# Performance work log

Hardware: AMD Instinct MI355X
Metric: run time of the kernel (lower is better)

## Reference

```python
import jax, jax.numpy as jnp
from jax import lax
import numpy as np

N_DFT = 1024
N_HOP = 256
N_FILTER = N_DFT // 2 + 1  # 513
AMIN = 1e-10
DYNAMIC_RANGE = 80.0


def _make_dft_kernels(n_dft):
    """Real/imag DFT kernels with periodic Hann window, shape (n_dft, 1, n_filter) for WIO conv."""
    nb = n_dft // 2 + 1
    t = np.arange(n_dft)
    w = np.arange(nb) * 2.0 * np.pi / float(n_dft)
    real = np.cos(w[:, None] * t[None, :])           # (nb, n_dft)
    imag = -np.sin(w[:, None] * t[None, :])
    # scipy periodic ('fftbins=True') hann window
    win = 0.5 - 0.5 * np.cos(2.0 * np.pi * t / float(n_dft))
    real = (real * win).T[:, None, :]                # (n_dft, 1, nb) = (W, I, O)
    imag = (imag * win).T[:, None, :]
    return real.astype(np.float32), imag.astype(np.float32)


def setup_inputs() -> dict:
    key = jax.random.key(0)
    x = jax.random.normal(key, (32, 2, 262144), dtype=jnp.float32)  # (batch, n_ch, len_src)
    kr, ki = _make_dft_kernels(N_DFT)
    return {"x": x, "k_real": jnp.asarray(kr), "k_imag": jnp.asarray(ki)}


def reference(x, k_real, k_imag):
    B, CH, L = x.shape
    xm = x.reshape(B * CH, L, 1)  # treat each audio channel as an independent mono signal
    dn = ("NWC", "WIO", "NWC")
    conv = lambda k: lax.conv_general_dilated(
        xm, k, window_strides=(N_HOP,), padding="SAME", dimension_numbers=dn
    )
    # power spectrogram: real^2 + imag^2 -> (B*CH, n_frame, n_filter)
    power = conv(k_real) ** 2 + conv(k_imag) ** 2
    n_frame = power.shape[1]
    # -> (B, n_filter, n_frame, CH)  (channels_last image format)
    spec = power.reshape(B, CH, n_frame, N_FILTER).transpose(0, 3, 2, 1)
    # power_spectrogram == 2.0, so no pow; return_decibel_spectrogram == True:
    log_spec = 10.0 * jnp.log10(jnp.maximum(spec, AMIN))
    log_spec = log_spec - jnp.max(log_spec, axis=(1, 2, 3), keepdims=True)
    return jnp.maximum(log_spec, -DYNAMIC_RANGE)
```

## Files before the change

### kernel.cpp

```cpp
#include <hip/hip_runtime.h>
#include <math.h>

namespace {
constexpr int NDFT   = 1024;
constexpr int NHOP   = 256;
constexpr int NFILT  = 513;
constexpr int LSRC   = 262144;
constexpr int NFRAME = 1024;
constexpr int PAD_L  = 384;
constexpr long PER_B = (long)NFILT * NFRAME * 2;

constexpr int KT2 = 16;
constexpr int CHUNK_US = 8192;
constexpr size_t WSB2_BYTES = (size_t)8 * KT2 * CHUNK_US * 2;
constexpr size_t PLANE_ELEMS_PER_SIG = 1024 * 512;

constexpr int KT1 = 32;
constexpr size_t WS_B_BYTES = (size_t)8 * KT1 * CHUNK_US * 2;
}

using short8 = __attribute__((ext_vector_type(8))) short;
using f32x4  = __attribute__((ext_vector_type(4))) float;

__device__ __forceinline__ unsigned int f2key(float f) {
    unsigned int u = __float_as_uint(f);
    return (u & 0x80000000u) ? ~u : (u | 0x80000000u);
}
__device__ __forceinline__ float key2f(unsigned int k) {
    return (k & 0x80000000u) ? __uint_as_float(k ^ 0x80000000u) : __uint_as_float(~k);
}
__device__ __forceinline__ unsigned short bf16rn(float v) {
    unsigned int u = __float_as_uint(v);
    return (unsigned short)((u + 0x7fffu + ((u >> 16) & 1u)) >> 16);
}

__global__ void zero_ws(unsigned int* __restrict__ w) {
    if (threadIdx.x < 32) w[threadIdx.x] = 0u;
}

__global__ __launch_bounds__(256) void fold_split(
    const float* __restrict__ x,
    unsigned short* __restrict__ sH, unsigned short* __restrict__ sL,
    unsigned short* __restrict__ dH, unsigned short* __restrict__ dL,
    int sig0)
{
    const int floc = blockIdx.x * 4 + (threadIdx.x >> 6);
    const int grp  = threadIdx.x & 63;
    const int sig  = sig0 + (floc >> 10);
    const int fl   = floc & 1023;
    const long sbase = (long)sig * LSRC;
    const int st   = fl * NHOP - PAD_L;
    const int s0   = grp * 8;

    const float xmid = x[sbase + st + 512];

    float fw[8], bw[8];
    if (fl >= 2 && fl <= 1021) {
        const float4 a0 = *reinterpret_cast<const float4*>(x + sbase + st + s0);
        const float4 a1 = *reinterpret_cast<const float4*>(x + sbase + st + s0 + 4);
        fw[0]=a0.x; fw[1]=a0.y; fw[2]=a0.z; fw[3]=a0.w;
        fw[4]=a1.x; fw[5]=a1.y; fw[6]=a1.z; fw[7]=a1.w;
        const long q0 = sbase + st + 1017 - s0;
        const float4 b0 = *reinterpret_cast<const float4*>(x + q0 - 1);
        const float4 b1 = *reinterpret_cast<const float4*>(x + q0 + 3);
        const float  b2 = x[q0 + 7];
        const float va[8] = {b0.y, b0.z, b0.w, b1.x, b1.y, b1.z, b1.w, b2};
        #pragma unroll
        for (int j = 0; j < 8; ++j) bw[j] = va[7 - j];
    } else {
        #pragma unroll
        for (int j = 0; j < 8; ++j) {
            const int s = s0 + j;
            const int p1 = st + s;
            const int p2 = st + 1024 - s;
            fw[j] = ((unsigned)p1 < (unsigned)LSRC) ? x[sbase + p1] : 0.0f;
            bw[j] = ((unsigned)p2 < (unsigned)LSRC) ? x[sbase + p2] : 0.0f;
        }
    }

    union { unsigned short u[8]; uint4 v; } shv, slv, dhv, dlv;
    #pragma unroll
    for (int j = 0; j < 8; ++j) {
        float x1 = fw[j], x2 = bw[j];
        if (j == 0 && s0 == 0) { x1 = xmid; x2 = 0.0f; }
        const float sm = x1 + x2;
        const float df = x1 - x2;
        const unsigned short h1 = bf16rn(sm);
        shv.u[j] = h1;
        slv.u[j] = bf16rn(sm - __uint_as_float((unsigned int)h1 << 16));
        const unsigned short h2 = bf16rn(df);
        dhv.u[j] = h2;
        dlv.u[j] = bf16rn(df - __uint_as_float((unsigned int)h2 << 16));
    }
    const size_t wo = (size_t)floc * 512 + s0;
    *reinterpret_cast<uint4*>(sH + wo) = shv.v;
    *reinterpret_cast<uint4*>(sL + wo) = slv.v;
    *reinterpret_cast<uint4*>(dH + wo) = dhv.v;
    *reinterpret_cast<uint4*>(dL + wo) = dlv.v;
}

__global__ __launch_bounds__(256) void build_B2(const float* __restrict__ kr,
                                                const float* __restrict__ ki,
                                                unsigned short* __restrict__ wsB)
{
    const int nt = blockIdx.x >> 4;
    const int kt = blockIdx.x & 15;
    unsigned short* chunk = wsB + (size_t)blockIdx.x * CHUNK_US;
    const int col = threadIdx.x >> 1;
    const int h   = threadIdx.x & 1;
    const int bin = nt * 64 + (col & 63);
    const float* src = (col < 64) ? kr : ki;
    #pragma unroll
    for (int j = 0; j < 4; ++j) {
        const int sl = h * 4 + j;
        const int c  = sl & 3;
        union { unsigned short u[8]; uint4 v; } pk;
        #pragma unroll
        for (int i = 0; i < 8; ++i) {
            const int s = kt * 32 + c * 8 + i;
            const int t = (s == 0) ? 512 : s;
            const float v = src[t * NFILT + bin];
            const unsigned short hi = bf16rn(v);
            pk.u[i] = h ? bf16rn(v - __uint_as_float((unsigned int)hi << 16)) : hi;
        }
        *reinterpret_cast<uint4*>(&chunk[col * 64 + ((sl ^ (col & 7)) << 3)]) = pk.v;
    }
}

__global__ __launch_bounds__(256, 2) void spec_gemm2(
    const unsigned short* __restrict__ sH, const unsigned short* __restrict__ sL,
    const unsigned short* __restrict__ dH, const unsigned short* __restrict__ dL,
    const unsigned short* __restrict__ wsB,
    float* __restrict__ out, unsigned int* __restrict__ wmax,
    int sig0, int nsig)
{
    __shared__ unsigned short smem[24576];

    const int tid  = threadIdx.x;
    const int lane = tid & 63, w = tid >> 6;
    const int wm = w & 1, wn = w >> 1;
    const int l15 = lane & 15, l16 = lane >> 4;

    const int phys = blockIdx.x;
    const int xcd  = phys & 7, slot = phys >> 3;
    const int nt   = slot & 7;
    const int mt   = xcd * nsig + (slot >> 3);
    const int sig  = sig0 + (mt >> 3);
    const int f0   = (mt & 7) * 128;
    const unsigned short* bchunks = wsB + (size_t)nt * KT2 * CHUNK_US;

    const unsigned short* __restrict__ pH = wn ? dH : sH;
    const unsigned short* __restrict__ pL = wn ? dL : sL;

    const int rl = lane >> 3, jj = lane & 7;
    const int q  = jj ^ rl;
    const unsigned short* apl = (q < 4) ? pH : pL;
    const unsigned short* agsrc[8];
    #pragma unroll
    for (int i = 0; i < 8; ++i)
        agsrc[i] = apl + (size_t)(mt * 128 + wm * 64 + i * 8 + rl) * 512 + (q & 3) * 8;

    unsigned short* Areg  = smem + wn * 12288;
    unsigned short* Breg  = Areg + 8192;
    unsigned short* aldst = Areg + wm * 4096;
    unsigned short* bldst = Breg + wm * 2048;

    f32x4 acc[4][4];
    #pragma unroll
    for (int i = 0; i < 4; ++i)
        #pragma unroll
        for (int j = 0; j < 4; ++j)
            #pragma unroll
            for (int r = 0; r < 4; ++r) acc[i][j][r] = 0.0f;

    #define STAGE(ktv)                                                         \
        {                                                                      \
            _Pragma("unroll")                                                  \
            for (int i = 0; i < 8; ++i)                                        \
                __builtin_amdgcn_global_load_lds(                              \
                    (const __attribute__((address_space(1))) unsigned int*)(agsrc[i] + (ktv) * 32), \
                    (__attribute__((address_space(3))) unsigned int*)(aldst + i * 512), \
                    16, 0, 0);                                                 \
            const unsigned short* gBs = bchunks + (size_t)(ktv) * CHUNK_US + wn * 4096 + wm * 2048; \
            _Pragma("unroll")                                                  \
            for (int i = 0; i < 4; ++i)                                        \
                __builtin_amdgcn_global_load_lds(                              \
                    (const __attribute__((address_space(1))) unsigned int*)(gBs + i * 512 + lane * 8), \
                    (__attribute__((address_space(3))) unsigned int*)(bldst + i * 512), \
                    16, 0, 0);                                                 \
        }

    #define COMPUTE()                                                          \
        {                                                                      \
            short8 ah[4], al[4], bh[4], bl[4];                                 \
            _Pragma("unroll")                                                  \
            for (int mf = 0; mf < 4; ++mf) {                                   \
                const int row = wm * 64 + mf * 16 + l15;                       \
                const unsigned short* ab = Areg + row * 64;                    \
                ah[mf] = *reinterpret_cast<const short8*>(ab + ((l16 ^ (row & 7)) << 3));        \
                al[mf] = *reinterpret_cast<const short8*>(ab + (((4 + l16) ^ (row & 7)) << 3));  \
            }                                                                  \
            _Pragma("unroll")                                                  \
            for (int nf = 0; nf < 4; ++nf) {                                   \
                const int coll = nf * 16 + l15;                                \
                const unsigned short* bb = Breg + coll * 64;                   \
                bh[nf] = *reinterpret_cast<const short8*>(bb + ((l16 ^ (coll & 7)) << 3));       \
                bl[nf] = *reinterpret_cast<const short8*>(bb + (((4 + l16) ^ (coll & 7)) << 3)); \
            }                                                                  \
            __builtin_amdgcn_s_setprio(1);                                     \
            _Pragma("unroll")                                                  \
            for (int nf = 0; nf < 4; ++nf)                                     \
                _Pragma("unroll")                                              \
                for (int mf = 0; mf < 4; ++mf) {                               \
                    acc[mf][nf] = __builtin_amdgcn_mfma_f32_16x16x32_bf16(ah[mf], bh[nf], acc[mf][nf], 0, 0, 0); \
                    acc[mf][nf] = __builtin_amdgcn_mfma_f32_16x16x32_bf16(al[mf], bh[nf], acc[mf][nf], 0, 0, 0); \
                    acc[mf][nf] = __builtin_amdgcn_mfma_f32_16x16x32_bf16(ah[mf], bl[nf], acc[mf][nf], 0, 0, 0); \
                }                                                              \
            __builtin_amdgcn_s_setprio(0);                                     \
        }

    #pragma unroll 1
    for (int kt = 0; kt < KT2; ++kt) {
        STAGE(kt)
        __syncthreads();
        COMPUTE()
        __syncthreads();
    }
    #undef STAGE
    #undef COMPUTE

    if (wn == 0) {
        #pragma unroll
        for (int mf = 0; mf < 4; ++mf)
            #pragma unroll
            for (int nf = 0; nf < 4; ++nf) {
                const int binl = nf * 16 + l15;
                #pragma unroll
                for (int r = 0; r < 4; ++r) {
                    const int row = wm * 64 + mf * 16 + l16 * 4 + r;
                    const float v = acc[mf][nf][r];
                    smem[row * 68 + binl] = bf16rn(v * v);
                }
            }
    }
    __syncthreads();
    if (wn == 1) {
        const int batch = sig >> 1, ch = sig & 1;
        float lmax = -3.0e38f;
        #pragma unroll
        for (int mf = 0; mf < 4; ++mf)
            #pragma unroll
            for (int nf = 0; nf < 4; ++nf) {
                const int binl = nf * 16 + l15;
                const int bin  = nt * 64 + binl;
                #pragma unroll
                for (int r = 0; r < 4; ++r) {
                    const int row = wm * 64 + mf * 16 + l16 * 4 + r;
                    const float v = acc[mf][nf][r];
                    const float re2 = __uint_as_float((unsigned int)smem[row * 68 + binl] << 16);
                    const float p = re2 + v * v;
                    const float d = 10.0f * log10f(fmaxf(p, 1e-10f));
                    const int frame = f0 + row;
                    out[((long)(batch * NFILT + bin) * NFRAME + frame) * 2 + ch] = d;
                    lmax = fmaxf(lmax, d);
                }
            }
        #pragma unroll
        for (int off = 32; off > 0; off >>= 1) lmax = fmaxf(lmax, __shfl_xor(lmax, off));
        if (lane == 0) atomicMax(&wmax[batch], f2key(lmax));
    }
}

__global__ __launch_bounds__(256) void build_B(const float* __restrict__ kr,
                                               const float* __restrict__ ki,
                                               unsigned short* __restrict__ wsB)
{
    const int nt = blockIdx.x >> 5;
    const int kt = blockIdx.x & 31;
    unsigned short* chunk = wsB + (size_t)blockIdx.x * CHUNK_US;
    const int col = threadIdx.x >> 1;
    const int h   = threadIdx.x & 1;
    const int bin = nt * 64 + (col >> 1);
    const float* src = (col & 1) ? ki : kr;
    #pragma unroll
    for (int j = 0; j < 4; ++j) {
        const int sl = h * 4 + j;
        const int c  = sl & 3;
        union { unsigned short u[8]; uint4 v; } pk;
        #pragma unroll
        for (int i = 0; i < 8; ++i) {
            const int t = kt * 32 + c * 8 + i;
            const float v = src[t * NFILT + bin];
            const unsigned short hi = bf16rn(v);
            pk.u[i] = h ? bf16rn(v - __uint_as_float((unsigned int)hi << 16)) : hi;
        }
        *reinterpret_cast<uint4*>(&chunk[col * 64 + ((sl ^ (col & 7)) << 3)]) = pk.v;
    }
}

__global__ __launch_bounds__(256, 2) void spec_gemm_mid(
    const float* __restrict__ x, const unsigned short* __restrict__ wsB,
    float* __restrict__ out, unsigned int* __restrict__ wmax)
{
    __shared__ unsigned short Ad[2][128][64];
    __shared__ unsigned short Bd[2][128][64];

    const int tid  = threadIdx.x;
    const int lane = tid & 63, w = tid >> 6;
    const int wm = w >> 1, wn = w & 1;
    const int l15 = lane & 15, l16 = lane >> 4;
    const int mt = blockIdx.x, nt = blockIdx.y;
    const int sig = mt >> 3, f0 = (mt & 7) * 128;
    const long sb = (long)sig * LSRC;

    const int arow = tid >> 1, ac2 = tid & 1;
    const int abase_p = (f0 + arow) * NHOP - PAD_L + ac2 * 16;
    const unsigned short* bchunks = wsB + (size_t)nt * KT1 * CHUNK_US;

    f32x4 acc[4][4];
    #pragma unroll
    for (int i = 0; i < 4; ++i)
        #pragma unroll
        for (int j = 0; j < 4; ++j)
            #pragma unroll
            for (int r = 0; r < 4; ++r) acc[i][j][r] = 0.0f;

    float va[16];

    #define LOAD_A(ktv)                                                        \
        {                                                                      \
            const int p0 = abase_p + (ktv) * 32;                               \
            if (p0 >= 0 && p0 + 16 <= LSRC) {                                  \
                *reinterpret_cast<float4*>(&va[0])  = *reinterpret_cast<const float4*>(x + sb + p0);      \
                *reinterpret_cast<float4*>(&va[4])  = *reinterpret_cast<const float4*>(x + sb + p0 + 4);  \
                *reinterpret_cast<float4*>(&va[8])  = *reinterpret_cast<const float4*>(x + sb + p0 + 8);  \
                *reinterpret_cast<float4*>(&va[12]) = *reinterpret_cast<const float4*>(x + sb + p0 + 12); \
            } else {                                                           \
                _Pragma("unroll")                                              \
                for (int i = 0; i < 16; ++i) {                                 \
                    const int p = p0 + i;                                      \
                    va[i] = (p >= 0 && p < LSRC) ? x[sb + p] : 0.0f;           \
                }                                                              \
            }                                                                  \
        }

    #define LOAD_B(ktv, nb)                                                    \
        {                                                                      \
            const char* g = (const char*)(bchunks + (size_t)(ktv) * CHUNK_US); \
            char* l = (char*)&Bd[nb][0][0];                                    \
            _Pragma("unroll")                                                  \
            for (int i = 0; i < 4; ++i) {                                      \
                const int off = i * 4096 + w * 1024;                           \
                __builtin_amdgcn_global_load_lds(                              \
                    (const __attribute__((address_space(1))) unsigned int*)(g + off + lane * 16), \
                    (__attribute__((address_space(3))) unsigned int*)(l + off), \
                    16, 0, 0);                                                 \
            }                                                                  \
        }

    #define WRITE_A(nb)                                                       \
        {                                                                      \
            unsigned short* ab = &Ad[nb][arow][0];                             \
            _Pragma("unroll")                                                  \
            for (int j = 0; j < 2; ++j) {                                      \
                union { unsigned short u[8]; uint4 v; } hv, lv;                \
                _Pragma("unroll")                                              \
                for (int i = 0; i < 8; ++i) {                                  \
                    const float vv = va[j * 8 + i];                            \
                    const unsigned short hi = bf16rn(vv);                      \
                    hv.u[i] = hi;                                              \
                    lv.u[i] = bf16rn(vv - __uint_as_float((unsigned int)hi << 16)); \
                }                                                              \
                const int c = ac2 * 2 + j;                                     \
                *reinterpret_cast<uint4*>(ab + (((c) ^ (arow & 7)) << 3))     = hv.v; \
                *reinterpret_cast<uint4*>(ab + (((4 + c) ^ (arow & 7)) << 3)) = lv.v; \
            }                                                                  \
        }

    LOAD_A(0)
    LOAD_B(0, 0)
    WRITE_A(0)
    __syncthreads();

    #pragma unroll 1
    for (int kt = 0; kt < KT1; ++kt) {
        const int cur = kt & 1, nxt = cur ^ 1;
        const bool pf = (kt + 1 < KT1);
        if (pf) {
            LOAD_A(kt + 1)
            LOAD_B(kt + 1, nxt)
        }
        short8 ah[4], al[4];
        #pragma unroll
        for (int mf = 0; mf < 4; ++mf) {
            const int row = wm * 64 + mf * 16 + l15;
            const unsigned short* ab = &Ad[cur][row][0];
            ah[mf] = *reinterpret_cast<const short8*>(ab + ((l16 ^ (row & 7)) << 3));
            al[mf] = *reinterpret_cast<const short8*>(ab + (((4 + l16) ^ (row & 7)) << 3));
        }
        __builtin_amdgcn_s_setprio(1);
        #pragma unroll
        for (int nf = 0; nf < 4; ++nf) {
            const int col = wn * 64 + nf * 16 + l15;
            const unsigned short* bb = &Bd[cur][col][0];
            const short8 bh = *reinterpret_cast<const short8*>(bb + ((l16 ^ (col & 7)) << 3));
            const short8 bl = *reinterpret_cast<const short8*>(bb + (((4 + l16) ^ (col & 7)) << 3));
            #pragma unroll
            for (int mf = 0; mf < 4; ++mf) {
                acc[mf][nf] = __builtin_amdgcn_mfma_f32_16x16x32_bf16(ah[mf], bh, acc[mf][nf], 0, 0, 0);
                acc[mf][nf] = __builtin_amdgcn_mfma_f32_16x16x32_bf16(al[mf], bh, acc[mf][nf], 0, 0, 0);
                acc[mf][nf] = __builtin_amdgcn_mfma_f32_16x16x32_bf16(ah[mf], bl, acc[mf][nf], 0, 0, 0);
            }
        }
        __builtin_amdgcn_s_setprio(0);
        if (pf) WRITE_A(nxt)
        __syncthreads();
    }
    #undef LOAD_A
    #undef LOAD_B
    #undef WRITE_A

    const int batch = sig >> 1, ch = sig & 1;
    float lmax = -3.0e38f;
    #pragma unroll
    for (int mf = 0; mf < 4; ++mf)
        #pragma unroll
        for (int nf = 0; nf < 4; ++nf) {
            const int col = nt * 128 + wn * 64 + nf * 16 + l15;
            const int bin = col >> 1;
            #pragma unroll
            for (int r = 0; r < 4; ++r) {
                const float v  = acc[mf][nf][r];
                const float sq = v * v;
                const float p  = sq + __shfl_xor(sq, 1);
                if (!(lane & 1)) {
                    const int frame = f0 + wm * 64 + mf * 16 + l16 * 4 + r;
                    const float d = 10.0f * log10f(fmaxf(p, 1e-10f));
                    out[((long)(batch * NFILT + bin) * NFRAME + frame) * 2 + ch] = d;
                    lmax = fmaxf(lmax, d);
                }
            }
        }
    #pragma unroll
    for (int off = 32; off > 0; off >>= 1) lmax = fmaxf(lmax, __shfl_xor(lmax, off));
    if (lane == 0) atomicMax(&wmax[batch], f2key(lmax));
}

__global__ __launch_bounds__(256, 2) void spec_nyq(
    const float* __restrict__ x, const float* __restrict__ kr,
    const float* __restrict__ ki, float* __restrict__ out,
    unsigned int* __restrict__ wmax)
{
    __shared__ float xs[17152];
    __shared__ float kc[1024], ks[1024];
    const int sig = blockIdx.x >> 4, ft = blockIdx.x & 15;
    const int f0 = ft * 64;
    const long sb = (long)sig * LSRC;
    const int start = f0 * NHOP - PAD_L;
    for (int i = threadIdx.x; i < 17152; i += 256) {
        const int p = start + i;
        xs[i] = (p >= 0 && p < LSRC) ? x[sb + p] : 0.0f;
    }
    for (int t = threadIdx.x; t < 1024; t += 256) {
        kc[t] = kr[t * NFILT + 512];
        ks[t] = ki[t * NFILT + 512];
    }
    __syncthreads();
    const int fr = threadIdx.x >> 2, q = threadIdx.x & 3;
    const int rot = ((fr + q) & 7) * 4;
    float re = 0.0f, im = 0.0f;
    #pragma unroll 4
    for (int j = 0; j < 256; j += 4) {
        const int je = (j + rot) & 255;
        const float4 a = *reinterpret_cast<const float4*>(&xs[fr * 256 + q * 256 + je]);
        const float4 c = *reinterpret_cast<const float4*>(&kc[q * 256 + je]);
        const float4 s = *reinterpret_cast<const float4*>(&ks[q * 256 + je]);
        re = fmaf(a.x, c.x, re); re = fmaf(a.y, c.y, re);
        re = fmaf(a.z, c.z, re); re = fmaf(a.w, c.w, re);
        im = fmaf(a.x, s.x, im); im = fmaf(a.y, s.y, im);
        im = fmaf(a.z, s.z, im); im = fmaf(a.w, s.w, im);
    }
    re += __shfl_xor(re, 1); re += __shfl_xor(re, 2);
    im += __shfl_xor(im, 1); im += __shfl_xor(im, 2);
    const int batch = sig >> 1, ch = sig & 1;
    float lmax = -3.0e38f;
    if (q == 0) {
        const float p = re * re + im * im;
        const float d = 10.0f * log10f(fmaxf(p, 1e-10f));
        out[((long)(batch * NFILT + 512) * NFRAME + (f0 + fr)) * 2 + ch] = d;
        lmax = d;
    }
    #pragma unroll
    for (int off = 32; off > 0; off >>= 1) lmax = fmaxf(lmax, __shfl_xor(lmax, off));
    if ((threadIdx.x & 63) == 0) atomicMax(&wmax[batch], f2key(lmax));
}

__global__ __launch_bounds__(256) void finalize(
    float* __restrict__ out, const unsigned int* __restrict__ wmax, long n4)
{
    const long stride = (long)gridDim.x * 256;
    for (long i4 = blockIdx.x * 256L + threadIdx.x; i4 < n4; i4 += stride) {
        const long i = i4 * 4;
        const int b  = (int)(i / PER_B);
        const float m = key2f(wmax[b]);
        float4 v = reinterpret_cast<float4*>(out)[i4];
        v.x = fmaxf(v.x - m, -80.0f);
        v.y = fmaxf(v.y - m, -80.0f);
        v.z = fmaxf(v.z - m, -80.0f);
        v.w = fmaxf(v.w - m, -80.0f);
        reinterpret_cast<float4*>(out)[i4] = v;
    }
}

namespace fb {
constexpr int TILE_F = 32;
constexpr int SPAN   = (TILE_F - 1) * NHOP + NDFT;
}

__global__ __launch_bounds__(256) void spec_main_fb(
    const float* __restrict__ x, const float* __restrict__ kr,
    const float* __restrict__ ki, float* __restrict__ out,
    unsigned int* __restrict__ wmax)
{
    __shared__ float xs[fb::SPAN];
    const int s   = blockIdx.x;
    const int f0  = blockIdx.y * fb::TILE_F;
    const int tid = threadIdx.x;
    const long sig_base = (long)s * LSRC;
    const int start = f0 * NHOP - PAD_L;
    for (int i = tid; i < fb::SPAN; i += 256) {
        const int p = start + i;
        xs[i] = (p >= 0 && p < LSRC) ? x[sig_base + p] : 0.0f;
    }
    __syncthreads();
    const int b0 = tid, b1 = tid + 256;
    float ar0[fb::TILE_F], ai0[fb::TILE_F], ar1[fb::TILE_F], ai1[fb::TILE_F];
    #pragma unroll
    for (int f = 0; f < fb::TILE_F; ++f) { ar0[f]=0.f; ai0[f]=0.f; ar1[f]=0.f; ai1[f]=0.f; }
    #pragma unroll 1
    for (int t = 0; t < NDFT; t += 4) {
        float br0[4], bq0[4], br1[4], bq1[4];
        #pragma unroll
        for (int j = 0; j < 4; ++j) {
            br0[j] = kr[(t + j) * NFILT + b0]; bq0[j] = ki[(t + j) * NFILT + b0];
            br1[j] = kr[(t + j) * NFILT + b1]; bq1[j] = ki[(t + j) * NFILT + b1];
        }
        #pragma unroll
        for (int f = 0; f < fb::TILE_F; ++f) {
            const float4 a = *reinterpret_cast<const float4*>(&xs[t + NHOP * f]);
            ar0[f]=fmaf(a.x,br0[0],ar0[f]); ar0[f]=fmaf(a.y,br0[1],ar0[f]);
            ar0[f]=fmaf(a.z,br0[2],ar0[f]); ar0[f]=fmaf(a.w,br0[3],ar0[f]);
            ai0[f]=fmaf(a.x,bq0[0],ai0[f]); ai0[f]=fmaf(a.y,bq0[1],ai0[f]);
            ai0[f]=fmaf(a.z,bq0[2],ai0[f]); ai0[f]=fmaf(a.w,bq0[3],ai0[f]);
            ar1[f]=fmaf(a.x,br1[0],ar1[f]); ar1[f]=fmaf(a.y,br1[1],ar1[f]);
            ar1[f]=fmaf(a.z,br1[2],ar1[f]); ar1[f]=fmaf(a.w,br1[3],ar1[f]);
            ai1[f]=fmaf(a.x,bq1[0],ai1[f]); ai1[f]=fmaf(a.y,bq1[1],ai1[f]);
            ai1[f]=fmaf(a.z,bq1[2],ai1[f]); ai1[f]=fmaf(a.w,bq1[3],ai1[f]);
        }
    }
    const int b = s >> 1, ch = s & 1;
    float lmax = -3.0e38f;
    #pragma unroll
    for (int f = 0; f < fb::TILE_F; ++f) {
        const int frame = f0 + f;
        const float p0 = ar0[f]*ar0[f] + ai0[f]*ai0[f];
        const float p1 = ar1[f]*ar1[f] + ai1[f]*ai1[f];
        const float d0 = 10.0f * log10f(fmaxf(p0, 1e-10f));
        const float d1 = 10.0f * log10f(fmaxf(p1, 1e-10f));
        lmax = fmaxf(lmax, fmaxf(d0, d1));
        out[((long)(b * NFILT + b0) * NFRAME + frame) * 2 + ch] = d0;
        out[((long)(b * NFILT + b1) * NFRAME + frame) * 2 + ch] = d1;
    }
    #pragma unroll
    for (int off = 32; off > 0; off >>= 1) lmax = fmaxf(lmax, __shfl_xor(lmax, off));
    if ((tid & 63) == 0) atomicMax(&wmax[b], f2key(lmax));
}

__global__ __launch_bounds__(256) void spec_nyq_fb(
    const float* __restrict__ x, const float* __restrict__ kr,
    const float* __restrict__ ki, float* __restrict__ out,
    unsigned int* __restrict__ wmax)
{
    const int gid   = blockIdx.x * 256 + threadIdx.x;
    const int s     = gid >> 10;
    const int frame = gid & 1023;
    const float* xp = x + (long)s * LSRC;
    const int start = frame * NHOP - PAD_L;
    float re = 0.f, im = 0.f;
    for (int t = 0; t < NDFT; ++t) {
        const int idx = start + t;
        const float a = (idx >= 0 && idx < LSRC) ? xp[idx] : 0.0f;
        re = fmaf(a, kr[t * NFILT + 512], re);
        im = fmaf(a, ki[t * NFILT + 512], im);
    }
    const float p = re * re + im * im;
    const float d = 10.0f * log10f(fmaxf(p, 1e-10f));
    const int b = s >> 1, ch = s & 1;
    out[((long)(b * NFILT + 512) * NFRAME + frame) * 2 + ch] = d;
    float lmax = d;
    #pragma unroll
    for (int off = 32; off > 0; off >>= 1) lmax = fmaxf(lmax, __shfl_xor(lmax, off));
    if ((threadIdx.x & 63) == 0) atomicMax(&wmax[b], f2key(lmax));
}

extern "C" void kernel_launch(void* const* d_in, const int* in_sizes, int n_in,
                              void* d_out, int out_size, void* d_ws, size_t ws_size,
                              hipStream_t stream) {
    const float* x  = (const float*)d_in[0];
    const float* kr = (const float*)d_in[1];
    const float* ki = (const float*)d_in[2];
    float* out = (float*)d_out;
    const long n4 = (long)out_size / 4;

    int nsig = 0;
    const int cands[4] = {64, 32, 16, 8};
    for (int c = 0; c < 4; ++c) {
        const size_t need = 128 + WSB2_BYTES + (size_t)cands[c] * 4 * 1048576;
        if (ws_size >= need) { nsig = cands[c]; break; }
    }

    if (nsig) {
        unsigned int* wmax   = (unsigned int*)d_ws;
        unsigned short* wsB2 = (unsigned short*)((char*)d_ws + 128);
        unsigned short* sH   = (unsigned short*)((char*)d_ws + 128 + WSB2_BYTES);
        const size_t pe = (size_t)nsig * PLANE_ELEMS_PER_SIG;
        unsigned short* sL = sH + pe;
        unsigned short* dH = sL + pe;
        unsigned short* dL = dH + pe;
        zero_ws<<<1, 64, 0, stream>>>(wmax);
        build_B2<<<128, 256, 0, stream>>>(kr, ki, wsB2);
        const int npass = 64 / nsig;
        for (int p = 0; p < npass; ++p) {
            fold_split<<<nsig * 256, 256, 0, stream>>>(x, sH, sL, dH, dL, p * nsig);
            spec_gemm2<<<nsig * 64, 256, 0, stream>>>(sH, sL, dH, dL, wsB2, out, wmax,
                                                      p * nsig, nsig);
        }
        spec_nyq<<<1024, 256, 0, stream>>>(x, kr, ki, out, wmax);
        finalize<<<2048, 256, 0, stream>>>(out, wmax, n4);
    } else if (ws_size >= WS_B_BYTES + 128) {
        unsigned short* wsB = (unsigned short*)d_ws;
        unsigned int* wmax  = (unsigned int*)((char*)d_ws + WS_B_BYTES);
        zero_ws<<<1, 64, 0, stream>>>(wmax);
        build_B<<<8 * KT1, 256, 0, stream>>>(kr, ki, wsB);
        spec_gemm_mid<<<dim3(512, 8), 256, 0, stream>>>(x, wsB, out, wmax);
        spec_nyq<<<1024, 256, 0, stream>>>(x, kr, ki, out, wmax);
        finalize<<<2048, 256, 0, stream>>>(out, wmax, n4);
    } else {
        unsigned int* wmax = (unsigned int*)d_ws;
        zero_ws<<<1, 64, 0, stream>>>(wmax);
        dim3 grid(64, NFRAME / fb::TILE_F);
        spec_main_fb<<<grid, 256, 0, stream>>>(x, kr, ki, out, wmax);
        spec_nyq_fb<<<(64 * NFRAME) / 256, 256, 0, stream>>>(x, kr, ki, out, wmax);
        finalize<<<2048, 256, 0, stream>>>(out, wmax, n4);
    }
}
```

Measured before the change: 540.3 us.

## Enlarge GEMM block to 1024 threads with 128x128 tiles and double-buffered LDS

Rewrites spec_gemm2 so each block uses 16 waves and covers 128 frames by 128 bins for both the real and imaginary halves, in place of 64 bins. The A tile loaded into LDS is therefore shared across twice as many bins. LDS staging is now double-buffered, so the next k-tile loads while the current one computes, which removes one barrier per iteration. The trade-off is 128KB of shared memory and one block per CU, which lowers occupancy and leaves fewer, larger blocks.

New measurement: 567.7 us. +5.1%, slower.

```diff
diff --git a/kernel.cpp b/kernel.cpp
--- a/kernel.cpp
+++ b/kernel.cpp
@@ -127,27 +127,28 @@
     }
 }
 
-__global__ __launch_bounds__(256, 2) void spec_gemm2(
+__global__ __launch_bounds__(1024, 1) void spec_gemm2(
     const unsigned short* __restrict__ sH, const unsigned short* __restrict__ sL,
     const unsigned short* __restrict__ dH, const unsigned short* __restrict__ dL,
     const unsigned short* __restrict__ wsB,
     float* __restrict__ out, unsigned int* __restrict__ wmax,
     int sig0, int nsig)
 {
-    __shared__ unsigned short smem[24576];
+    __shared__ unsigned short smem[65536];
 
     const int tid  = threadIdx.x;
     const int lane = tid & 63, w = tid >> 6;
-    const int wm = w & 1, wn = w >> 1;
+    const int wn  = w >> 3;
+    const int aw  = w & 7;
+    const int mq  = aw >> 1, nh = aw & 1;
     const int l15 = lane & 15, l16 = lane >> 4;
 
     const int phys = blockIdx.x;
     const int xcd  = phys & 7, slot = phys >> 3;
-    const int nt   = slot & 7;
-    const int mt   = xcd * nsig + (slot >> 3);
+    const int ntp  = slot & 3;
+    const int mt   = xcd * nsig + (slot >> 2);
     const int sig  = sig0 + (mt >> 3);
     const int f0   = (mt & 7) * 128;
-    const unsigned short* bchunks = wsB + (size_t)nt * KT2 * CHUNK_US;
 
     const unsigned short* __restrict__ pH = wn ? dH : sH;
     const unsigned short* __restrict__ pL = wn ? dL : sL;
@@ -155,63 +156,70 @@
     const int rl = lane >> 3, jj = lane & 7;
     const int q  = jj ^ rl;
     const unsigned short* apl = (q < 4) ? pH : pL;
-    const unsigned short* agsrc[8];
-    #pragma unroll
-    for (int i = 0; i < 8; ++i)
-        agsrc[i] = apl + (size_t)(mt * 128 + wm * 64 + i * 8 + rl) * 512 + (q & 3) * 8;
-
-    unsigned short* Areg  = smem + wn * 12288;
-    unsigned short* Breg  = Areg + 8192;
-    unsigned short* aldst = Areg + wm * 4096;
-    unsigned short* bldst = Breg + wm * 2048;
-
-    f32x4 acc[4][4];
-    #pragma unroll
-    for (int i = 0; i < 4; ++i)
+    const unsigned short* agsrc[2];
+    #pragma unroll
+    for (int i = 0; i < 2; ++i)
+        agsrc[i] = apl + (size_t)(mt * 128 + aw * 16 + i * 8 + rl) * 512 + (q & 3) * 8;
+
+    const unsigned short* bgsrc[2];
+    #pragma unroll
+    for (int i = 0; i < 2; ++i) {
+        const int c = aw * 16 + i * 8 + rl;
+        const int ntg = ntp * 2 + (c >> 6);
+        bgsrc[i] = wsB + (size_t)(ntg * KT2) * CHUNK_US
+                 + (wn * 64 + (c & 63)) * 64 + jj * 8;
+    }
+
+    f32x4 acc[2][4];
+    #pragma unroll
+    for (int i = 0; i < 2; ++i)
         #pragma unroll
         for (int j = 0; j < 4; ++j)
             #pragma unroll
             for (int r = 0; r < 4; ++r) acc[i][j][r] = 0.0f;
 
-    #define STAGE(ktv)                                                         \
+    #define STAGE(ktv, buf)                                                    \
         {                                                                      \
+            unsigned short* abase_l = smem + (buf) * 32768 + wn * 8192 + aw * 1024; \
             _Pragma("unroll")                                                  \
-            for (int i = 0; i < 8; ++i)                                        \
+            for (int i = 0; i < 2; ++i)                                        \
                 __builtin_amdgcn_global_load_lds(                              \
-                    (const __attribute__((address_space(1))) unsigned int*)(agsrc[i] + (ktv) * 32), \
-                    (__attribute__((address_space(3))) unsigned int*)(aldst + i * 512), \
+                    (const __attribute__((address_space(1))) unsigned int*)(agsrc[i] + (size_t)(ktv) * 32), \
+                    (__attribute__((address_space(3))) unsigned int*)(abase_l + i * 512), \
                     16, 0, 0);                                                 \
-            const unsigned short* gBs = bchunks + (size_t)(ktv) * CHUNK_US + wn * 4096 + wm * 2048; \
+            unsigned short* bbase_l = smem + (buf) * 32768 + 16384 + wn * 8192 + aw * 1024; \
             _Pragma("unroll")                                                  \
-            for (int i = 0; i < 4; ++i)                                        \
+            for (int i = 0; i < 2; ++i)                                        \
                 __builtin_amdgcn_global_load_lds(                              \
-                    (const __attribute__((address_space(1))) unsigned int*)(gBs + i * 512 + lane * 8), \
-                    (__attribute__((address_space(3))) unsigned int*)(bldst + i * 512), \
+                    (const __attribute__((address_space(1))) unsigned int*)(bgsrc[i] + (size_t)(ktv) * CHUNK_US), \
+                    (__attribute__((address_space(3))) unsigned int*)(bbase_l + i * 512), \
                     16, 0, 0);                                                 \
         }
 
-    #define COMPUTE()                                                          \
+    #define COMPUTE(buf)                                                       \
         {                                                                      \
-            short8 ah[4], al[4], bh[4], bl[4];                                 \
+            const unsigned short* Areg = smem + (buf) * 32768 + wn * 8192;     \
+            const unsigned short* Breg = smem + (buf) * 32768 + 16384 + wn * 8192; \
+            short8 ah[2], al[2], bh[4], bl[4];                                 \
             _Pragma("unroll")                                                  \
-            for (int mf = 0; mf < 4; ++mf) {                                   \
-                const int row = wm * 64 + mf * 16 + l15;                       \
+            for (int mf = 0; mf < 2; ++mf) {                                   \
+                const int row = mq * 32 + mf * 16 + l15;                       \
                 const unsigned short* ab = Areg + row * 64;                    \
                 ah[mf] = *reinterpret_cast<const short8*>(ab + ((l16 ^ (row & 7)) << 3));        \
                 al[mf] = *reinterpret_cast<const short8*>(ab + (((4 + l16) ^ (row & 7)) << 3));  \
             }                                                                  \
             _Pragma("unroll")                                                  \
             for (int nf = 0; nf < 4; ++nf) {                                   \
-                const int coll = nf * 16 + l15;                                \
-                const unsigned short* bb = Breg + coll * 64;                   \
-                bh[nf] = *reinterpret_cast<const short8*>(bb + ((l16 ^ (coll & 7)) << 3));       \
-                bl[nf] = *reinterpret_cast<const short8*>(bb + (((4 + l16) ^ (coll & 7)) << 3)); \
+                const int c = nh * 64 + nf * 16 + l15;                         \
+                const unsigned short* bb = Breg + c * 64;                      \
+                bh[nf] = *reinterpret_cast<const short8*>(bb + ((l16 ^ (c & 7)) << 3));          \
+                bl[nf] = *reinterpret_cast<const short8*>(bb + (((4 + l16) ^ (c & 7)) << 3));    \
             }                                                                  \
             __builtin_amdgcn_s_setprio(1);                                     \
             _Pragma("unroll")                                                  \
             for (int nf = 0; nf < 4; ++nf)                                     \
                 _Pragma("unroll")                                              \
-                for (int mf = 0; mf < 4; ++mf) {                               \
+                for (int mf = 0; mf < 2; ++mf) {                               \
                     acc[mf][nf] = __builtin_amdgcn_mfma_f32_16x16x32_bf16(ah[mf], bh[nf], acc[mf][nf], 0, 0, 0); \
                     acc[mf][nf] = __builtin_amdgcn_mfma_f32_16x16x32_bf16(al[mf], bh[nf], acc[mf][nf], 0, 0, 0); \
                     acc[mf][nf] = __builtin_amdgcn_mfma_f32_16x16x32_bf16(ah[mf], bl[nf], acc[mf][nf], 0, 0, 0); \
@@ -219,11 +227,13 @@
             __builtin_amdgcn_s_setprio(0);                                     \
         }
 
+    STAGE(0, 0)
+    __syncthreads();
+
     #pragma unroll 1
     for (int kt = 0; kt < KT2; ++kt) {
-        STAGE(kt)
-        __syncthreads();
-        COMPUTE()
+        if (kt + 1 < KT2) STAGE(kt + 1, (kt + 1) & 1)
+        COMPUTE(kt & 1)
         __syncthreads();
     }
     #undef STAGE
@@ -231,15 +241,15 @@
 
     if (wn == 0) {
         #pragma unroll
-        for (int mf = 0; mf < 4; ++mf)
+        for (int mf = 0; mf < 2; ++mf)
             #pragma unroll
             for (int nf = 0; nf < 4; ++nf) {
-                const int binl = nf * 16 + l15;
+                const int c = nh * 64 + nf * 16 + l15;
                 #pragma unroll
                 for (int r = 0; r < 4; ++r) {
-                    const int row = wm * 64 + mf * 16 + l16 * 4 + r;
+                    const int row = mq * 32 + mf * 16 + l16 * 4 + r;
                     const float v = acc[mf][nf][r];
-                    smem[row * 68 + binl] = bf16rn(v * v);
+                    smem[row * 132 + c] = bf16rn(v * v);
                 }
             }
     }
@@ -248,16 +258,16 @@
         const int batch = sig >> 1, ch = sig & 1;
         float lmax = -3.0e38f;
         #pragma unroll
-        for (int mf = 0; mf < 4; ++mf)
+        for (int mf = 0; mf < 2; ++mf)
             #pragma unroll
             for (int nf = 0; nf < 4; ++nf) {
-                const int binl = nf * 16 + l15;
-                const int bin  = nt * 64 + binl;
+                const int c = nh * 64 + nf * 16 + l15;
+                const int bin = ntp * 128 + c;
                 #pragma unroll
                 for (int r = 0; r < 4; ++r) {
-                    const int row = wm * 64 + mf * 16 + l16 * 4 + r;
+                    const int row = mq * 32 + mf * 16 + l16 * 4 + r;
                     const float v = acc[mf][nf][r];
-                    const float re2 = __uint_as_float((unsigned int)smem[row * 68 + binl] << 16);
+                    const float re2 = __uint_as_float((unsigned int)smem[row * 132 + c] << 16);
                     const float p = re2 + v * v;
                     const float d = 10.0f * log10f(fmaxf(p, 1e-10f));
                     const int frame = f0 + row;
@@ -632,8 +642,8 @@
         const int npass = 64 / nsig;
         for (int p = 0; p < npass; ++p) {
             fold_split<<<nsig * 256, 256, 0, stream>>>(x, sH, sL, dH, dL, p * nsig);
-            spec_gemm2<<<nsig * 64, 256, 0, stream>>>(sH, sL, dH, dL, wsB2, out, wmax,
-                                                      p * nsig, nsig);
+            spec_gemm2<<<nsig * 32, 1024, 0, stream>>>(sH, sL, dH, dL, wsB2, out, wmax,
+                                                       p * nsig, nsig);
         }
         spec_nyq<<<1024, 256, 0, stream>>>(x, kr, ki, out, wmax);
         finalize<<<2048, 256, 0, stream>>>(out, wmax, n4);
```
